# Optimization experiments

Measured on AMD Instinct MI355X. Metric: run time of the kernel, lower is better.

Reference implementation:

```python
import jax, jax.numpy as jnp
import numpy as np

N_NODES = 1500
N_EDGES = 12000
IN_FEAT = 512
HIDDEN = 64
OUT_FEAT = 32
HEADS = 8
NEG_SLOPE = 0.2  # DGL GATConv default leaky_relu slope


def setup_inputs() -> dict:
    key = jax.random.key(0)
    ks = jax.random.split(key, 16)

    def xav(k, shape, fan_in):
        return jax.random.normal(k, shape, jnp.float32) * (1.0 / np.sqrt(fan_in))

    return {
        "node": jax.random.normal(ks[0], (N_NODES, IN_FEAT), jnp.float32),
        "src": jax.random.randint(ks[1], (N_EDGES,), 0, N_NODES, jnp.int32),
        "dst": jax.random.randint(ks[2], (N_EDGES,), 0, N_NODES, jnp.int32),
        "W1": xav(ks[3], (IN_FEAT, HEADS * HIDDEN), IN_FEAT),
        "al1": xav(ks[4], (HEADS, HIDDEN), HIDDEN),
        "ar1": xav(ks[5], (HEADS, HIDDEN), HIDDEN),
        "b1": jnp.zeros((HEADS, HIDDEN), jnp.float32),
        "W2": xav(ks[6], (HIDDEN, HEADS * HIDDEN), HIDDEN),
        "al2": xav(ks[7], (HEADS, HIDDEN), HIDDEN),
        "ar2": xav(ks[8], (HEADS, HIDDEN), HIDDEN),
        "b2": jnp.zeros((HEADS, HIDDEN), jnp.float32),
        "W3": xav(ks[9], (HIDDEN, HEADS * OUT_FEAT), HIDDEN),
        "al3": xav(ks[10], (HEADS, OUT_FEAT), OUT_FEAT),
        "ar3": xav(ks[11], (HEADS, OUT_FEAT), OUT_FEAT),
        "b3": jnp.zeros((HEADS, OUT_FEAT), jnp.float32),
    }


def gat_layer(h, W, al, ar, b, src, dst, n_nodes):
    """DGL GATConv semantics: h has shape [N, *prefix, F_in]; output [N, *prefix, H, F_out]."""
    H, Fo = al.shape
    feat = (h @ W).reshape(h.shape[:-1] + (H, Fo))          # [N, *P, H, Fo]
    el = (feat * al).sum(-1)                                 # [N, *P, H]
    er = (feat * ar).sum(-1)                                 # [N, *P, H]
    e = jax.nn.leaky_relu(el[src] + er[dst], NEG_SLOPE)      # [E, *P, H]
    # numerically stable edge softmax over incoming edges of each dst node
    emax = jax.lax.stop_gradient(jax.ops.segment_max(e, dst, num_segments=n_nodes))
    ex = jnp.exp(e - emax[dst])
    den = jax.ops.segment_sum(ex, dst, num_segments=n_nodes)
    a = ex / den[dst]                                        # [E, *P, H]
    msg = a[..., None] * feat[src]                           # [E, *P, H, Fo]
    return jax.ops.segment_sum(msg, dst, num_segments=n_nodes) + b


def reference(node, src, dst, W1, al1, ar1, b1, W2, al2, ar2, b2, W3, al3, ar3, b3):
    n = node.shape[0]
    h = gat_layer(node, W1, al1, ar1, b1, src, dst, n)       # [N, 8, 64]
    h = jax.nn.gelu(h, approximate=False)
    h = gat_layer(h, W2, al2, ar2, b2, src, dst, n)          # [N, 8, 8, 64]
    h = jax.nn.gelu(h, approximate=False)
    return gat_layer(h, W3, al3, ar3, b3, src, dst, n)       # [N, 8, 8, 8, 32]
```

## Files before the change

kernel.cpp:

```cpp
#include <hip/hip_runtime.h>
#include <math.h>

#define N_NODES 1500
#define N_EDGES 12000
#define IN_FEAT 512
#define HIDDEN 64
#define OUT_FEAT 32
#define HEADS 8

typedef short bf16x8 __attribute__((ext_vector_type(8)));
typedef float f32x4 __attribute__((ext_vector_type(4)));

__device__ __forceinline__ unsigned short f2bf(float f) {
    unsigned u = __float_as_uint(f);
    u += 0x7fff + ((u >> 16) & 1);
    return (unsigned short)(u >> 16);
}
__device__ __forceinline__ float bf2f(unsigned short b) {
    return __uint_as_float(((unsigned)b) << 16);
}
__device__ __forceinline__ unsigned packbf(float a) {
    unsigned short hi = f2bf(a);
    unsigned short lo = f2bf(a - bf2f(hi));
    return (unsigned)hi | ((unsigned)lo << 16);
}
__device__ __forceinline__ float rdlane(float v, int c) {
    return __uint_as_float(__builtin_amdgcn_readlane(__float_as_uint(v), c));
}


__global__ void prep_kernel(const float* __restrict__ W2, const float* __restrict__ al2,
                            const float* __restrict__ ar2,
                            const float* __restrict__ W3, const float* __restrict__ al3,
                            const float* __restrict__ ar3,
                            float* __restrict__ aleff2, float* __restrict__ areff2,
                            float* __restrict__ aleff3, float* __restrict__ areff3,
                            float* __restrict__ W4t2, unsigned* __restrict__ wfrag3,
                            int* __restrict__ counts, int* __restrict__ cursor) {
    int i = blockIdx.x * blockDim.x + threadIdx.x;
    if (i < 1536) {
        if (i < N_NODES + 1) counts[i] = 0;
        return;
    }
    i -= 1536;
    if (i < 1536) {
        if (i < N_NODES) cursor[i] = 0;
        return;
    }
    i -= 1536;
    if (i < 1024) {
        int lr = i >> 9; i &= 511;
        int h = i >> 6, k = i & 63;
        const float* a = lr ? ar2 : al2;
        float s = 0.f;
        for (int f = 0; f < 64; ++f)
            s = fmaf(W2[(size_t)k * 512 + h * 64 + f], a[h * 64 + f], s);
        (lr ? areff2 : aleff2)[h * 64 + k] = s;
        return;
    }
    i -= 1024;
    if (i < 1024) {
        int lr = i >> 9; i &= 511;
        int h = i >> 6, k = i & 63;
        const float* a = lr ? ar3 : al3;
        float s = 0.f;
        for (int f = 0; f < 32; ++f)
            s = fmaf(W3[(size_t)k * 256 + h * 32 + f], a[h * 32 + f], s);
        (lr ? areff3 : aleff3)[h * 64 + k] = s;
        return;
    }
    i -= 1024;
    if (i < 16 * 512 * 4) {
        int kg = i >> 11, rem = i & 2047;
        int c = rem >> 2, j = rem & 3;
        W4t2[i] = W2[(size_t)(kg * 4 + j) * 512 + c];
        return;
    }
    i -= 16 * 512 * 4;
    if (i < 16384) {
        int j = i & 7, l = (i >> 3) & 63;
        int ks = (i >> 9) & 1, nt = (i >> 10) & 1, h = (i >> 11) & 7;
        int k = ks * 32 + (l >> 4) * 8 + j;
        int col = h * 32 + nt * 16 + (l & 15);
        wfrag3[i] = packbf(W3[(size_t)k * 256 + col]);
    }
}

__global__ void hist_kernel(const int* __restrict__ dst, int* __restrict__ counts) {
    int e = blockIdx.x * blockDim.x + threadIdx.x;
    if (e < N_EDGES) atomicAdd(&counts[dst[e]], 1);
}

__global__ void scan_kernel(const int* __restrict__ counts, int* __restrict__ row_ptr) {
    __shared__ int part[256];
    int t = threadIdx.x;
    const int CH = (N_NODES + 255) / 256;
    int base = t * CH;
    int loc[8];
    int s = 0;
    for (int i = 0; i < CH; ++i) {
        int idx = base + i;
        int v = (idx < N_NODES) ? counts[idx] : 0;
        loc[i] = s;
        s += v;
    }
    part[t] = s;
    __syncthreads();
    if (t == 0) {
        int a = 0;
        for (int i = 0; i < 256; ++i) { int v = part[i]; part[i] = a; a += v; }
        row_ptr[N_NODES] = a;
    }
    __syncthreads();
    int p0 = part[t];
    for (int i = 0; i < CH; ++i) {
        int idx = base + i;
        if (idx < N_NODES) row_ptr[idx] = p0 + loc[i];
    }
}

__global__ void scatter_kernel(const int* __restrict__ dst, const int* __restrict__ row_ptr,
                               int* __restrict__ cursor, int* __restrict__ tmp_eid) {
    int e = blockIdx.x * blockDim.x + threadIdx.x;
    if (e < N_EDGES) {
        int d = dst[e];
        int pos = row_ptr[d] + atomicAdd(&cursor[d], 1);
        tmp_eid[pos] = e;
    }
}

__global__ void sort_csr_kernel(const int* __restrict__ row_ptr, const int* __restrict__ tmp_eid,
                                const int* __restrict__ src, int* __restrict__ csr_src) {
    int wid = (blockIdx.x * blockDim.x + threadIdx.x) >> 6;
    int lane = threadIdx.x & 63;
    if (wid >= N_NODES) return;
    int r0 = row_ptr[wid], deg = row_ptr[wid + 1] - r0;
    for (int base = 0; base < deg; base += 64) {
        int i = base + lane;
        int my = (i < deg) ? tmp_eid[r0 + i] : 0x7fffffff;
        int rank = 0;
        for (int b2 = 0; b2 < deg; b2 += 64) {
            int other = (b2 + lane < deg) ? tmp_eid[r0 + b2 + lane] : 0x7fffffff;
            int cnt2 = min(deg - b2, 64);
            for (int j = 0; j < cnt2; ++j) {
                int oj = __shfl(other, j);
                rank += (oj < my) ? 1 : 0;
            }
        }
        if (i < deg) csr_src[r0 + rank] = src[my];
    }
}


#define GM 32
#define GN 32
#define GK 32

__global__ __launch_bounds__(256) void gemm_f32(const float* __restrict__ A,
                                                const float* __restrict__ B,
                                                float* __restrict__ C,
                                                int M, int N, int K) {
    __shared__ float As[GK][GM + 2];
    __shared__ float Bs[GK][GN + 2];
    int t = threadIdx.x;
    int col0 = blockIdx.x * GN, row0 = blockIdx.y * GM;
    int tx = t & 15, ty = t >> 4;
    int am = t >> 3, ak = (t & 7) * 4;
    int bk = t >> 3, bn = (t & 7) * 4;
    float acc[2][2] = {};
    for (int k0 = 0; k0 < K; k0 += GK) {
        int gr = row0 + am;
        float4 av = (gr < M) ? *(const float4*)&A[(size_t)gr * K + k0 + ak]
                             : make_float4(0.f, 0.f, 0.f, 0.f);
        float4 bv = *(const float4*)&B[(size_t)(k0 + bk) * N + col0 + bn];
        __syncthreads();
        As[ak + 0][am] = av.x; As[ak + 1][am] = av.y;
        As[ak + 2][am] = av.z; As[ak + 3][am] = av.w;
        *(float4*)&Bs[bk][bn] = bv;
        __syncthreads();
        #pragma unroll
        for (int kk = 0; kk < GK; ++kk) {
            float2 a2 = *(const float2*)&As[kk][ty * 2];
            float2 b2 = *(const float2*)&Bs[kk][tx * 2];
            acc[0][0] = fmaf(a2.x, b2.x, acc[0][0]);
            acc[0][1] = fmaf(a2.x, b2.y, acc[0][1]);
            acc[1][0] = fmaf(a2.y, b2.x, acc[1][0]);
            acc[1][1] = fmaf(a2.y, b2.y, acc[1][1]);
        }
    }
    #pragma unroll
    for (int i = 0; i < 2; ++i) {
        int gr = row0 + ty * 2 + i;
        if (gr < M) {
            float2 v = make_float2(acc[i][0], acc[i][1]);
            *(float2*)&C[(size_t)gr * N + col0 + tx * 2] = v;
        }
    }
}


__global__ void elr_feat_kernel(const float* __restrict__ feat, const float* __restrict__ al,
                                const float* __restrict__ ar, float* __restrict__ el,
                                float* __restrict__ er, int RH) {
    int idx = blockIdx.x * blockDim.x + threadIdx.x;
    if (idx >= RH) return;
    int h = idx & (HEADS - 1);
    const float* fp = feat + (size_t)idx * HIDDEN;
    float sl = 0.f, sr = 0.f;
    for (int f = 0; f < HIDDEN; ++f) {
        float v = fp[f];
        sl = fmaf(v, al[h * HIDDEN + f], sl);
        sr = fmaf(v, ar[h * HIDDEN + f], sr);
    }
    el[idx] = sl;
    er[idx] = sr;
}

__global__ void elr_row_kernel(const float* __restrict__ X, const float* __restrict__ alv,
                               const float* __restrict__ arv, float* __restrict__ el,
                               float* __restrict__ er, int R) {
    int r = blockIdx.x * blockDim.x + threadIdx.x;
    if (r >= R) return;
    const float4* x4 = (const float4*)(X + (size_t)r * 64);
    float sl[8] = {}, sr[8] = {};
    for (int kg = 0; kg < 16; ++kg) {
        float4 xv = x4[kg];
        #pragma unroll
        for (int h = 0; h < 8; ++h) {
            float4 a = *(const float4*)&alv[h * 64 + kg * 4];
            float4 b = *(const float4*)&arv[h * 64 + kg * 4];
            sl[h] = fmaf(xv.x, a.x, fmaf(xv.y, a.y, fmaf(xv.z, a.z, fmaf(xv.w, a.w, sl[h]))));
            sr[h] = fmaf(xv.x, b.x, fmaf(xv.y, b.y, fmaf(xv.z, b.z, fmaf(xv.w, b.w, sr[h]))));
        }
    }
    float* elp = el + (size_t)r * 8;
    float* erp = er + (size_t)r * 8;
    #pragma unroll
    for (int h = 0; h < 8; ++h) { elp[h] = sl[h]; erp[h] = sr[h]; }
}

__device__ __forceinline__ float gelu_exact(float v) {
    return 0.5f * v * (1.0f + erff(v * 0.70710678118654752440f));
}

__global__ __launch_bounds__(256) void agg_l1(
    const float* __restrict__ feat, const float* __restrict__ el, const float* __restrict__ er,
    const float* __restrict__ bias, const int* __restrict__ row_ptr,
    const int* __restrict__ csr_src, float* __restrict__ out) {
    int n = blockIdx.x;
    int t = threadIdx.x, wv = t >> 6, lane = t & 63;
    int h0 = 2 * wv;
    int r0 = row_ptr[n], deg = row_ptr[n + 1] - r0;
    float2 erv = *(const float2*)&er[n * 8 + h0];
    float den0 = 0.f, den1 = 0.f, a0 = 0.f, a1 = 0.f;
    for (int i = 0; i < deg; ++i) {
        int s = csr_src[r0 + i];
        float2 elv = *(const float2*)&el[s * 8 + h0];
        float x0 = feat[((size_t)s * 8 + h0) * 64 + lane];
        float x1 = feat[((size_t)s * 8 + h0 + 1) * 64 + lane];
        float e0 = elv.x + erv.x; e0 = e0 > 0.f ? e0 : 0.2f * e0;
        float e1 = elv.y + erv.y; e1 = e1 > 0.f ? e1 : 0.2f * e1;
        float w0 = __expf(e0), w1 = __expf(e1);
        den0 += w0; den1 += w1;
        a0 = fmaf(w0, x0, a0);
        a1 = fmaf(w1, x1, a1);
    }
    float i0 = deg ? 1.f / den0 : 0.f;
    float i1 = deg ? 1.f / den1 : 0.f;
    float v0 = a0 * i0 + bias[h0 * 64 + lane];
    float v1 = a1 * i1 + bias[(h0 + 1) * 64 + lane];
    out[((size_t)n * 8 + h0) * 64 + lane] = gelu_exact(v0);
    out[((size_t)n * 8 + h0 + 1) * 64 + lane] = gelu_exact(v1);
}

template <int FOUT, bool GELU, int P>
__global__ __launch_bounds__(256, 4) void agg_fused4(
    const float* __restrict__ X,
    const float* __restrict__ el, const float* __restrict__ er,
    const float* __restrict__ W4t,
    const float* __restrict__ bias,
    const int* __restrict__ row_ptr, const int* __restrict__ csr_src,
    float* __restrict__ out)
{
    constexpr int TOT = 8 * FOUT;
    constexpr int KSPLIT = 2;
    constexpr int KGPT = 8;
    constexpr int FELEM = (FOUT == 32) ? 2 : 4;
    constexpr int FQn = FOUT / FELEM;
    constexpr int TPK = 8 * FQn;
    constexpr int FQ4 = FOUT / 4;
    constexpr int PTS = FOUT + 4;
    constexpr int WPFL = (KSPLIT * 64 * PTS > 64 * 64) ? KSPLIT * 64 * PTS : 64 * 64;
    constexpr int GRPS = P / 8;
    constexpr int CHUNK = 64;

    int nb = blockIdx.x;
    int n = nb / GRPS, pg = nb - n * GRPS;
    int p0 = pg * 8;
    int r0 = row_ptr[n], deg = row_ptr[n + 1] - r0;
    int t = threadIdx.x, wv = t >> 6, lane = t & 63;

    __shared__ int src_s[CHUNK];
    __shared__ float inv_s[64];
    __shared__ float acc_s[8][8][68];
    __shared__ float wp_lds[WPFL];

    float agg0[8], agg1[8];
    #pragma unroll
    for (int h = 0; h < 8; ++h) { agg0[h] = 0.f; agg1[h] = 0.f; }
    float den = 0.f;

    int elbase_n = (n * P + p0) * 8;
    int pA = p0 + wv * 2;

    for (int c0 = 0; c0 < deg; c0 += CHUNK) {
        int cnt = min(deg - c0, CHUNK);
        __syncthreads();
        if (t < cnt) src_s[t] = csr_src[r0 + c0 + t];
        for (int j = t; j < cnt * 64; j += 256) {
            int i = j >> 6, plh = j & 63;
            int s = csr_src[r0 + c0 + i];
            float e = el[(s * P + p0) * 8 + plh] + er[elbase_n + plh];
            e = e > 0.f ? e : 0.2f * e;
            wp_lds[i * 64 + plh] = __expf(e);
        }
        __syncthreads();
        if (t < 64) {
            for (int i = 0; i < cnt; ++i) den += wp_lds[i * 64 + t];
        }
        auto edge_fma = [&](int i) {
            int s = src_s[i];
            const float* wp = &wp_lds[i * 64 + wv * 16];
            float4 w0 = *(const float4*)wp;
            float4 w1 = *(const float4*)(wp + 4);
            float4 w2 = *(const float4*)(wp + 8);
            float4 w3 = *(const float4*)(wp + 12);
            int xb = (s * P + pA) * 64 + lane;
            float xv0 = X[xb];
            float xv1 = X[xb + 64];
            agg0[0] = fmaf(w0.x, xv0, agg0[0]);
            agg0[1] = fmaf(w0.y, xv0, agg0[1]);
            agg0[2] = fmaf(w0.z, xv0, agg0[2]);
            agg0[3] = fmaf(w0.w, xv0, agg0[3]);
            agg0[4] = fmaf(w1.x, xv0, agg0[4]);
            agg0[5] = fmaf(w1.y, xv0, agg0[5]);
            agg0[6] = fmaf(w1.z, xv0, agg0[6]);
            agg0[7] = fmaf(w1.w, xv0, agg0[7]);
            agg1[0] = fmaf(w2.x, xv1, agg1[0]);
            agg1[1] = fmaf(w2.y, xv1, agg1[1]);
            agg1[2] = fmaf(w2.z, xv1, agg1[2]);
            agg1[3] = fmaf(w2.w, xv1, agg1[3]);
            agg1[4] = fmaf(w3.x, xv1, agg1[4]);
            agg1[5] = fmaf(w3.y, xv1, agg1[5]);
            agg1[6] = fmaf(w3.z, xv1, agg1[6]);
            agg1[7] = fmaf(w3.w, xv1, agg1[7]);
        };
        int i = 0;
        for (; i + 2 <= cnt; i += 2) { edge_fma(i); edge_fma(i + 1); }
        if (i < cnt) edge_fma(i);
    }
    if (t < 64) inv_s[t] = deg ? 1.f / den : 0.f;
    __syncthreads();
    {
        int pl0 = wv * 2;
        #pragma unroll
        for (int h = 0; h < 8; ++h) {
            acc_s[pl0][h][lane] = agg0[h] * inv_s[pl0 * 8 + h];
            acc_s[pl0 + 1][h][lane] = agg1[h] * inv_s[pl0 * 8 + 8 + h];
        }
    }
    __syncthreads();

    {
        int kq = t / TPK;
        int rem = t - kq * TPK;
        int h = rem / FQn;
        int ft = rem - h * FQn;
        int f0 = ft * FELEM;
        float part[8][FELEM];
        #pragma unroll
        for (int pl = 0; pl < 8; ++pl)
            #pragma unroll
            for (int j = 0; j < FELEM; ++j) part[pl][j] = 0.f;
        #pragma unroll
        for (int kk = 0; kk < KGPT; ++kk) {
            int kg = kq * KGPT + kk;
            float4 wr[FELEM];
            #pragma unroll
            for (int j = 0; j < FELEM; ++j)
                wr[j] = *(const float4*)&W4t[(size_t)(kg * TOT + h * FOUT + f0 + j) * 4];
            #pragma unroll
            for (int pl = 0; pl < 8; ++pl) {
                float4 a4 = *(const float4*)&acc_s[pl][h][kg * 4];
                #pragma unroll
                for (int j = 0; j < FELEM; ++j)
                    part[pl][j] = fmaf(a4.x, wr[j].x, fmaf(a4.y, wr[j].y,
                                  fmaf(a4.z, wr[j].z, fmaf(a4.w, wr[j].w, part[pl][j]))));
            }
        }
        #pragma unroll
        for (int pl = 0; pl < 8; ++pl) {
            float* dstp = &wp_lds[((kq * 8 + pl) * 8 + h) * PTS + f0];
            if (FELEM == 4)
                *(float4*)dstp = make_float4(part[pl][0], part[pl][1], part[pl][2], part[pl][3]);
            else
                *(float2*)dstp = make_float2(part[pl][0], part[pl][1]);
        }
    }
    __syncthreads();

    {
        constexpr int NQ = 2 * TOT;
        for (int q = t; q < NQ; q += 256) {
            int pl = q / (TOT / 4);
            int rem = q - pl * (TOT / 4);
            int h = rem / FQ4, fq = rem - h * FQ4;
            int f0 = fq * 4;
            float4 acc4 = *(const float4*)&wp_lds[((0 * 8 + pl) * 8 + h) * PTS + f0];
            #pragma unroll
            for (int kq = 1; kq < KSPLIT; ++kq) {
                float4 pv = *(const float4*)&wp_lds[((kq * 8 + pl) * 8 + h) * PTS + f0];
                acc4.x += pv.x; acc4.y += pv.y; acc4.z += pv.z; acc4.w += pv.w;
            }
            float4 b4 = *(const float4*)&bias[h * FOUT + f0];
            acc4.x += b4.x; acc4.y += b4.y; acc4.z += b4.z; acc4.w += b4.w;
            if (GELU) {
                acc4.x = gelu_exact(acc4.x); acc4.y = gelu_exact(acc4.y);
                acc4.z = gelu_exact(acc4.z); acc4.w = gelu_exact(acc4.w);
            }
            *(float4*)&out[(size_t)(n * P + p0 + pl) * TOT + h * FOUT + f0] = acc4;
        }
    }
}

__global__ __launch_bounds__(256, 4) void agg_mfma5(
    const float* __restrict__ X,
    const float* __restrict__ el, const float* __restrict__ er,
    const unsigned* __restrict__ wfrag,
    const float* __restrict__ bias,
    const int* __restrict__ row_ptr, const int* __restrict__ csr_src,
    float* __restrict__ out)
{
    int nb = blockIdx.x;
    int n = nb >> 2, pg = nb & 3;
    int p0 = pg * 16;
    int r0 = row_ptr[n], deg = row_ptr[n + 1] - r0;
    int t = threadIdx.x, wv = t >> 6, lane = t & 63;
    int pA = p0 + wv * 4;

    __shared__ unsigned accP[8][16][68];

    int c = lane & 31;
    float erv = er[(n * 64 + pA) * 8 + c];

    float agg[4][8];
    #pragma unroll
    for (int q = 0; q < 4; ++q)
        #pragma unroll
        for (int h = 0; h < 8; ++h) agg[q][h] = 0.f;
    float den_half = 0.f;

    for (int it = 0; it < deg; it += 2) {
        int s0 = csr_src[r0 + it];
        bool v1 = (it + 1 < deg);
        int s1 = v1 ? csr_src[r0 + it + 1] : s0;
        int sw = (lane < 32) ? s0 : s1;
        float e = el[(sw * 64 + pA) * 8 + c] + erv;
        e = e > 0.f ? e : 0.2f * e;
        if (lane >= 32 && !v1) e = -1e30f;
        float w = __expf(e);
        den_half += w;
        int xb0 = (s0 * 64 + pA) * 64 + lane;
        int xb1 = (s1 * 64 + pA) * 64 + lane;
        float xv0[4], xv1[4];
        #pragma unroll
        for (int q = 0; q < 4; ++q) xv0[q] = X[xb0 + q * 64];
        #pragma unroll
        for (int q = 0; q < 4; ++q) xv1[q] = X[xb1 + q * 64];
        #pragma unroll
        for (int q = 0; q < 4; ++q) {
            #pragma unroll
            for (int h = 0; h < 8; ++h) {
                float w0 = rdlane(w, q * 8 + h);
                float w1 = rdlane(w, 32 + q * 8 + h);
                agg[q][h] = fmaf(w0, xv0[q], agg[q][h]);
                agg[q][h] = fmaf(w1, xv1[q], agg[q][h]);
            }
        }
    }
    float den = den_half + __shfl(den_half, lane ^ 32);
    float inv = deg ? 1.f / den : 0.f;

    #pragma unroll
    for (int q = 0; q < 4; ++q) {
        int pl = wv * 4 + q;
        #pragma unroll
        for (int h = 0; h < 8; ++h) {
            float iv = rdlane(inv, q * 8 + h);
            accP[h][pl][lane] = packbf(agg[q][h] * iv);
        }
    }
    __syncthreads();

    int m16 = lane & 15, g = lane >> 4;
    #pragma unroll
    for (int hh = 0; hh < 2; ++hh) {
        int h = wv * 2 + hh;
        bf16x8 a_hi[2], a_lo[2];
        #pragma unroll
        for (int ks = 0; ks < 2; ++ks) {
            const unsigned* ap = &accP[h][m16][ks * 32 + g * 8];
            uint4 q0 = *(const uint4*)ap;
            uint4 q1 = *(const uint4*)(ap + 4);
            a_hi[ks][0] = (short)(q0.x & 0xffffu); a_lo[ks][0] = (short)(q0.x >> 16);
            a_hi[ks][1] = (short)(q0.y & 0xffffu); a_lo[ks][1] = (short)(q0.y >> 16);
            a_hi[ks][2] = (short)(q0.z & 0xffffu); a_lo[ks][2] = (short)(q0.z >> 16);
            a_hi[ks][3] = (short)(q0.w & 0xffffu); a_lo[ks][3] = (short)(q0.w >> 16);
            a_hi[ks][4] = (short)(q1.x & 0xffffu); a_lo[ks][4] = (short)(q1.x >> 16);
            a_hi[ks][5] = (short)(q1.y & 0xffffu); a_lo[ks][5] = (short)(q1.y >> 16);
            a_hi[ks][6] = (short)(q1.z & 0xffffu); a_lo[ks][6] = (short)(q1.z >> 16);
            a_hi[ks][7] = (short)(q1.w & 0xffffu); a_lo[ks][7] = (short)(q1.w >> 16);
        }
        #pragma unroll
        for (int nt = 0; nt < 2; ++nt) {
            f32x4 D = {0.f, 0.f, 0.f, 0.f};
            #pragma unroll
            for (int ks = 0; ks < 2; ++ks) {
                const unsigned* bp = &wfrag[(size_t)(((h * 2 + nt) * 2 + ks) * 64 + lane) * 8];
                uint4 w0 = *(const uint4*)bp;
                uint4 w1 = *(const uint4*)(bp + 4);
                bf16x8 b_hi, b_lo;
                b_hi[0] = (short)(w0.x & 0xffffu); b_lo[0] = (short)(w0.x >> 16);
                b_hi[1] = (short)(w0.y & 0xffffu); b_lo[1] = (short)(w0.y >> 16);
                b_hi[2] = (short)(w0.z & 0xffffu); b_lo[2] = (short)(w0.z >> 16);
                b_hi[3] = (short)(w0.w & 0xffffu); b_lo[3] = (short)(w0.w >> 16);
                b_hi[4] = (short)(w1.x & 0xffffu); b_lo[4] = (short)(w1.x >> 16);
                b_hi[5] = (short)(w1.y & 0xffffu); b_lo[5] = (short)(w1.y >> 16);
                b_hi[6] = (short)(w1.z & 0xffffu); b_lo[6] = (short)(w1.z >> 16);
                b_hi[7] = (short)(w1.w & 0xffffu); b_lo[7] = (short)(w1.w >> 16);
                D = __builtin_amdgcn_mfma_f32_16x16x32_bf16(a_hi[ks], b_hi, D, 0, 0, 0);
                D = __builtin_amdgcn_mfma_f32_16x16x32_bf16(a_hi[ks], b_lo, D, 0, 0, 0);
                D = __builtin_amdgcn_mfma_f32_16x16x32_bf16(a_lo[ks], b_hi, D, 0, 0, 0);
            }
            float bv = bias[h * 32 + nt * 16 + m16];
            size_t ob = ((size_t)(n * 64) + p0 + g * 4) * 256 + h * 32 + nt * 16 + m16;
            out[ob]       = D[0] + bv;
            out[ob + 256] = D[1] + bv;
            out[ob + 512] = D[2] + bv;
            out[ob + 768] = D[3] + bv;
        }
    }
}


extern "C" void kernel_launch(void* const* d_in, const int* in_sizes, int n_in,
                              void* d_out, int out_size, void* d_ws, size_t ws_size,
                              hipStream_t stream) {
    const float* node = (const float*)d_in[0];
    const int* src = (const int*)d_in[1];
    const int* dst = (const int*)d_in[2];
    const float* W1 = (const float*)d_in[3];
    const float* al1 = (const float*)d_in[4];
    const float* ar1 = (const float*)d_in[5];
    const float* b1 = (const float*)d_in[6];
    const float* W2 = (const float*)d_in[7];
    const float* al2 = (const float*)d_in[8];
    const float* ar2 = (const float*)d_in[9];
    const float* b2 = (const float*)d_in[10];
    const float* W3 = (const float*)d_in[11];
    const float* al3 = (const float*)d_in[12];
    const float* ar3 = (const float*)d_in[13];
    const float* b3 = (const float*)d_in[14];
    float* out = (float*)d_out;

    char* ws = (char*)d_ws;
    size_t off = 0;
    auto alloc = [&](size_t nb) -> char* {
        char* q = ws + off;
        off += (nb + 255) & ~(size_t)255;
        return q;
    };
    int* counts   = (int*)alloc((N_NODES + 1) * sizeof(int));
    int* cursor   = (int*)alloc(N_NODES * sizeof(int));
    int* row_ptr  = (int*)alloc((N_NODES + 1) * sizeof(int));
    int* tmp_eid  = (int*)alloc(N_EDGES * sizeof(int));
    int* csr_src  = (int*)alloc(N_EDGES * sizeof(int));
    float* feat1  = (float*)alloc((size_t)N_NODES * 8 * 64 * 4);
    float* el1    = (float*)alloc((size_t)N_NODES * 8 * 4);
    float* er1    = (float*)alloc((size_t)N_NODES * 8 * 4);
    float* h1     = (float*)alloc((size_t)N_NODES * 8 * 64 * 4);
    float* aleff2 = (float*)alloc(8 * 64 * 4);
    float* areff2 = (float*)alloc(8 * 64 * 4);
    float* el2    = (float*)alloc((size_t)N_NODES * 8 * 8 * 4);
    float* er2    = (float*)alloc((size_t)N_NODES * 8 * 8 * 4);
    float* h2     = (float*)alloc((size_t)N_NODES * 64 * 64 * 4);
    float* aleff3 = (float*)alloc(8 * 64 * 4);
    float* areff3 = (float*)alloc(8 * 64 * 4);
    float* el3    = (float*)alloc((size_t)N_NODES * 64 * 8 * 4);
    float* er3    = (float*)alloc((size_t)N_NODES * 64 * 8 * 4);
    float* W4t2   = (float*)alloc((size_t)16 * 512 * 4 * 4);
    unsigned* wfrag3 = (unsigned*)alloc((size_t)16384 * 4);

    const int PREP_T = 1536 + 1536 + 1024 + 1024 + 16 * 512 * 4 + 16384;
    prep_kernel<<<(PREP_T + 255) / 256, 256, 0, stream>>>(
        W2, al2, ar2, W3, al3, ar3, aleff2, areff2, aleff3, areff3, W4t2, wfrag3,
        counts, cursor);

    hist_kernel<<<(N_EDGES + 255) / 256, 256, 0, stream>>>(dst, counts);
    scan_kernel<<<1, 256, 0, stream>>>(counts, row_ptr);
    scatter_kernel<<<(N_EDGES + 255) / 256, 256, 0, stream>>>(dst, row_ptr, cursor, tmp_eid);
    sort_csr_kernel<<<(N_NODES * 64 + 255) / 256, 256, 0, stream>>>(row_ptr, tmp_eid, src, csr_src);

    dim3 g1((512 + GN - 1) / GN, (N_NODES + GM - 1) / GM);
    gemm_f32<<<g1, 256, 0, stream>>>(node, W1, feat1, N_NODES, 512, IN_FEAT);
    elr_feat_kernel<<<(N_NODES * 8 + 255) / 256, 256, 0, stream>>>(feat1, al1, ar1, el1, er1, N_NODES * 8);
    agg_l1<<<N_NODES, 256, 0, stream>>>(feat1, el1, er1, b1, row_ptr, csr_src, h1);

    elr_row_kernel<<<(N_NODES * 8 + 255) / 256, 256, 0, stream>>>(h1, aleff2, areff2, el2, er2, N_NODES * 8);
    agg_fused4<64, true, 8><<<N_NODES, 256, 0, stream>>>(h1, el2, er2, W4t2, b2, row_ptr, csr_src, h2);

    elr_row_kernel<<<(N_NODES * 64 + 255) / 256, 256, 0, stream>>>(h2, aleff3, areff3, el3, er3, N_NODES * 64);
    agg_mfma5<<<N_NODES * 4, 256, 0, stream>>>(h2, el3, er3, wfrag3, b3, row_ptr, csr_src, out);
}
```

Before: 177.4 us.

## Wave-register edge index broadcast, 4-edge unrolling, split bf16 weight planes, block remap

All three aggregation kernels now load a chunk of up to 64 source indices into one register per lane and broadcast them with readlane, replacing repeated global or LDS index loads. The layer-3 aggregation processes four edges per iteration so more gathers are in flight. Its B fragments now come as pre-split hi/lo bf16 planes and load directly as vectors, with no unpacking in the kernel. Block indices are remapped so that consecutive blocks handle different p-groups. The extra unrolling raises register pressure, and the remap changes L2 locality in ways that are hard to predict.

```diff
diff --git a/kernel.cpp b/kernel.cpp
--- a/kernel.cpp
+++ b/kernel.cpp
@@ -24,7 +24,7 @@
     unsigned short lo = f2bf(a - bf2f(hi));
     return (unsigned)hi | ((unsigned)lo << 16);
 }
-__device__ __forceinline__ float rdlane(float v, int c) {
+__device__ __forceinline__ float rdlanef(float v, int c) {
     return __uint_as_float(__builtin_amdgcn_readlane(__float_as_uint(v), c));
 }
 
@@ -35,7 +35,8 @@
                             const float* __restrict__ ar3,
                             float* __restrict__ aleff2, float* __restrict__ areff2,
                             float* __restrict__ aleff3, float* __restrict__ areff3,
-                            float* __restrict__ W4t2, unsigned* __restrict__ wfrag3,
+                            float* __restrict__ W4t2,
+                            unsigned* __restrict__ wfhi, unsigned* __restrict__ wflo,
                             int* __restrict__ counts, int* __restrict__ cursor) {
     int i = blockIdx.x * blockDim.x + threadIdx.x;
     if (i < 1536) {
@@ -78,11 +79,21 @@
     }
     i -= 16 * 512 * 4;
     if (i < 16384) {
-        int j = i & 7, l = (i >> 3) & 63;
-        int ks = (i >> 9) & 1, nt = (i >> 10) & 1, h = (i >> 11) & 7;
-        int k = ks * 32 + (l >> 4) * 8 + j;
+        int plane = i >> 13;
+        int rem = i & 8191;
+        int j2 = rem & 3, l = (rem >> 2) & 63;
+        int ks = (rem >> 8) & 1, nt = (rem >> 9) & 1, h = (rem >> 10) & 7;
         int col = h * 32 + nt * 16 + (l & 15);
-        wfrag3[i] = packbf(W3[(size_t)k * 256 + col]);
+        int kb = ks * 32 + (l >> 4) * 8 + 2 * j2;
+        unsigned parts[2];
+        #pragma unroll
+        for (int q = 0; q < 2; ++q) {
+            float w = W3[(size_t)(kb + q) * 256 + col];
+            unsigned short hi = f2bf(w);
+            parts[q] = plane ? (unsigned)f2bf(w - bf2f(hi)) : (unsigned)hi;
+        }
+        unsigned word = parts[0] | (parts[1] << 16);
+        (plane ? wflo : wfhi)[rem] = word;
     }
 }
 
@@ -253,17 +264,28 @@
     int r0 = row_ptr[n], deg = row_ptr[n + 1] - r0;
     float2 erv = *(const float2*)&er[n * 8 + h0];
     float den0 = 0.f, den1 = 0.f, a0 = 0.f, a1 = 0.f;
-    for (int i = 0; i < deg; ++i) {
-        int s = csr_src[r0 + i];
-        float2 elv = *(const float2*)&el[s * 8 + h0];
-        float x0 = feat[((size_t)s * 8 + h0) * 64 + lane];
-        float x1 = feat[((size_t)s * 8 + h0 + 1) * 64 + lane];
-        float e0 = elv.x + erv.x; e0 = e0 > 0.f ? e0 : 0.2f * e0;
-        float e1 = elv.y + erv.y; e1 = e1 > 0.f ? e1 : 0.2f * e1;
-        float w0 = __expf(e0), w1 = __expf(e1);
-        den0 += w0; den1 += w1;
-        a0 = fmaf(w0, x0, a0);
-        a1 = fmaf(w1, x1, a1);
+    for (int c0 = 0; c0 < deg; c0 += 64) {
+        int cnt = min(deg - c0, 64);
+        int src_r = (lane < cnt) ? csr_src[r0 + c0 + lane] : 0;
+        auto do_edge = [&](int s) {
+            float2 elv = *(const float2*)&el[s * 8 + h0];
+            float x0 = feat[((size_t)s * 8 + h0) * 64 + lane];
+            float x1 = feat[((size_t)s * 8 + h0 + 1) * 64 + lane];
+            float e0 = elv.x + erv.x; e0 = e0 > 0.f ? e0 : 0.2f * e0;
+            float e1 = elv.y + erv.y; e1 = e1 > 0.f ? e1 : 0.2f * e1;
+            float w0 = __expf(e0), w1 = __expf(e1);
+            den0 += w0; den1 += w1;
+            a0 = fmaf(w0, x0, a0);
+            a1 = fmaf(w1, x1, a1);
+        };
+        int i = 0;
+        for (; i + 2 <= cnt; i += 2) {
+            int s0 = __builtin_amdgcn_readlane(src_r, i);
+            int s1 = __builtin_amdgcn_readlane(src_r, i + 1);
+            do_edge(s0);
+            do_edge(s1);
+        }
+        if (i < cnt) do_edge(__builtin_amdgcn_readlane(src_r, i));
     }
     float i0 = deg ? 1.f / den0 : 0.f;
     float i1 = deg ? 1.f / den1 : 0.f;
@@ -300,7 +322,6 @@
     int r0 = row_ptr[n], deg = row_ptr[n + 1] - r0;
     int t = threadIdx.x, wv = t >> 6, lane = t & 63;
 
-    __shared__ int src_s[CHUNK];
     __shared__ float inv_s[64];
     __shared__ float acc_s[8][8][68];
     __shared__ float wp_lds[WPFL];
@@ -312,24 +333,25 @@
 
     int elbase_n = (n * P + p0) * 8;
     int pA = p0 + wv * 2;
+    float erv_t = er[elbase_n + lane];
 
     for (int c0 = 0; c0 < deg; c0 += CHUNK) {
         int cnt = min(deg - c0, CHUNK);
+        int src_r = (lane < cnt) ? csr_src[r0 + c0 + lane] : 0;
         __syncthreads();
-        if (t < cnt) src_s[t] = csr_src[r0 + c0 + t];
         for (int j = t; j < cnt * 64; j += 256) {
-            int i = j >> 6, plh = j & 63;
-            int s = csr_src[r0 + c0 + i];
-            float e = el[(s * P + p0) * 8 + plh] + er[elbase_n + plh];
+            int i = j >> 6;
+            int s = __builtin_amdgcn_readlane(src_r, i);
+            float e = el[(s * P + p0) * 8 + lane] + erv_t;
             e = e > 0.f ? e : 0.2f * e;
-            wp_lds[i * 64 + plh] = __expf(e);
+            wp_lds[i * 64 + lane] = __expf(e);
         }
         __syncthreads();
         if (t < 64) {
             for (int i = 0; i < cnt; ++i) den += wp_lds[i * 64 + t];
         }
         auto edge_fma = [&](int i) {
-            int s = src_s[i];
+            int s = __builtin_amdgcn_readlane(src_r, i);
             const float* wp = &wp_lds[i * 64 + wv * 16];
             float4 w0 = *(const float4*)wp;
             float4 w1 = *(const float4*)(wp + 4);
@@ -436,13 +458,14 @@
 __global__ __launch_bounds__(256, 4) void agg_mfma5(
     const float* __restrict__ X,
     const float* __restrict__ el, const float* __restrict__ er,
-    const unsigned* __restrict__ wfrag,
+    const unsigned* __restrict__ wfhi, const unsigned* __restrict__ wflo,
     const float* __restrict__ bias,
     const int* __restrict__ row_ptr, const int* __restrict__ csr_src,
     float* __restrict__ out)
 {
-    int nb = blockIdx.x;
-    int n = nb >> 2, pg = nb & 3;
+    int b = blockIdx.x;
+    int w = (b & 7) * 750 + (b >> 3);
+    int pg = w / N_NODES, n = w - pg * N_NODES;
     int p0 = pg * 16;
     int r0 = row_ptr[n], deg = row_ptr[n + 1] - r0;
     int t = threadIdx.x, wv = t >> 6, lane = t & 63;
@@ -460,31 +483,49 @@
         for (int h = 0; h < 8; ++h) agg[q][h] = 0.f;
     float den_half = 0.f;
 
-    for (int it = 0; it < deg; it += 2) {
-        int s0 = csr_src[r0 + it];
-        bool v1 = (it + 1 < deg);
-        int s1 = v1 ? csr_src[r0 + it + 1] : s0;
-        int sw = (lane < 32) ? s0 : s1;
-        float e = el[(sw * 64 + pA) * 8 + c] + erv;
-        e = e > 0.f ? e : 0.2f * e;
-        if (lane >= 32 && !v1) e = -1e30f;
-        float w = __expf(e);
-        den_half += w;
-        int xb0 = (s0 * 64 + pA) * 64 + lane;
-        int xb1 = (s1 * 64 + pA) * 64 + lane;
-        float xv0[4], xv1[4];
-        #pragma unroll
-        for (int q = 0; q < 4; ++q) xv0[q] = X[xb0 + q * 64];
-        #pragma unroll
-        for (int q = 0; q < 4; ++q) xv1[q] = X[xb1 + q * 64];
-        #pragma unroll
-        for (int q = 0; q < 4; ++q) {
-            #pragma unroll
-            for (int h = 0; h < 8; ++h) {
-                float w0 = rdlane(w, q * 8 + h);
-                float w1 = rdlane(w, 32 + q * 8 + h);
-                agg[q][h] = fmaf(w0, xv0[q], agg[q][h]);
-                agg[q][h] = fmaf(w1, xv1[q], agg[q][h]);
+    for (int c0 = 0; c0 < deg; c0 += 64) {
+        int cnt = min(deg - c0, 64);
+        int src_r = (lane < cnt) ? csr_src[r0 + c0 + lane] : 0;
+        for (int it = 0; it < cnt; it += 4) {
+            int i1 = min(it + 1, cnt - 1), i2 = min(it + 2, cnt - 1), i3 = min(it + 3, cnt - 1);
+            int s0 = __builtin_amdgcn_readlane(src_r, it);
+            int s1 = __builtin_amdgcn_readlane(src_r, i1);
+            int s2 = __builtin_amdgcn_readlane(src_r, i2);
+            int s3 = __builtin_amdgcn_readlane(src_r, i3);
+            bool v1 = it + 1 < cnt, v2 = it + 2 < cnt, v3 = it + 3 < cnt;
+            int sA = (lane < 32) ? s0 : s1;
+            int sB = (lane < 32) ? s2 : s3;
+            float eA = el[(sA * 64 + pA) * 8 + c] + erv;
+            float eB = el[(sB * 64 + pA) * 8 + c] + erv;
+            eA = eA > 0.f ? eA : 0.2f * eA;
+            eB = eB > 0.f ? eB : 0.2f * eB;
+            if (lane >= 32 && !v1) eA = -1e30f;
+            if (lane < 32 && !v2) eB = -1e30f;
+            if (lane >= 32 && !v3) eB = -1e30f;
+            float wA = __expf(eA), wB = __expf(eB);
+            den_half += wA + wB;
+            int xb0 = (s0 * 64 + pA) * 64 + lane;
+            int xb1 = (s1 * 64 + pA) * 64 + lane;
+            int xb2 = (s2 * 64 + pA) * 64 + lane;
+            int xb3 = (s3 * 64 + pA) * 64 + lane;
+            float x0[4], x1[4], x2[4], x3[4];
+            #pragma unroll
+            for (int q = 0; q < 4; ++q) x0[q] = X[xb0 + q * 64];
+            #pragma unroll
+            for (int q = 0; q < 4; ++q) x1[q] = X[xb1 + q * 64];
+            #pragma unroll
+            for (int q = 0; q < 4; ++q) x2[q] = X[xb2 + q * 64];
+            #pragma unroll
+            for (int q = 0; q < 4; ++q) x3[q] = X[xb3 + q * 64];
+            #pragma unroll
+            for (int q = 0; q < 4; ++q) {
+                #pragma unroll
+                for (int h = 0; h < 8; ++h) {
+                    agg[q][h] = fmaf(rdlanef(wA, q * 8 + h), x0[q], agg[q][h]);
+                    agg[q][h] = fmaf(rdlanef(wA, 32 + q * 8 + h), x1[q], agg[q][h]);
+                    agg[q][h] = fmaf(rdlanef(wB, q * 8 + h), x2[q], agg[q][h]);
+                    agg[q][h] = fmaf(rdlanef(wB, 32 + q * 8 + h), x3[q], agg[q][h]);
+                }
             }
         }
     }
@@ -496,7 +537,7 @@
         int pl = wv * 4 + q;
         #pragma unroll
         for (int h = 0; h < 8; ++h) {
-            float iv = rdlane(inv, q * 8 + h);
+            float iv = rdlanef(inv, q * 8 + h);
             accP[h][pl][lane] = packbf(agg[q][h] * iv);
         }
     }
@@ -526,18 +567,9 @@
             f32x4 D = {0.f, 0.f, 0.f, 0.f};
             #pragma unroll
             for (int ks = 0; ks < 2; ++ks) {
-                const unsigned* bp = &wfrag[(size_t)(((h * 2 + nt) * 2 + ks) * 64 + lane) * 8];
-                uint4 w0 = *(const uint4*)bp;
-                uint4 w1 = *(const uint4*)(bp + 4);
-                bf16x8 b_hi, b_lo;
-                b_hi[0] = (short)(w0.x & 0xffffu); b_lo[0] = (short)(w0.x >> 16);
-                b_hi[1] = (short)(w0.y & 0xffffu); b_lo[1] = (short)(w0.y >> 16);
-                b_hi[2] = (short)(w0.z & 0xffffu); b_lo[2] = (short)(w0.z >> 16);
-                b_hi[3] = (short)(w0.w & 0xffffu); b_lo[3] = (short)(w0.w >> 16);
-                b_hi[4] = (short)(w1.x & 0xffffu); b_lo[4] = (short)(w1.x >> 16);
-                b_hi[5] = (short)(w1.y & 0xffffu); b_lo[5] = (short)(w1.y >> 16);
-                b_hi[6] = (short)(w1.z & 0xffffu); b_lo[6] = (short)(w1.z >> 16);
-                b_hi[7] = (short)(w1.w & 0xffffu); b_lo[7] = (short)(w1.w >> 16);
+                size_t fb = (size_t)(((h * 2 + nt) * 2 + ks) * 64 + lane) * 4;
+                bf16x8 b_hi = *(const bf16x8*)&wfhi[fb];
+                bf16x8 b_lo = *(const bf16x8*)&wflo[fb];
                 D = __builtin_amdgcn_mfma_f32_16x16x32_bf16(a_hi[ks], b_hi, D, 0, 0, 0);
                 D = __builtin_amdgcn_mfma_f32_16x16x32_bf16(a_hi[ks], b_lo, D, 0, 0, 0);
                 D = __builtin_amdgcn_mfma_f32_16x16x32_bf16(a_lo[ks], b_hi, D, 0, 0, 0);
@@ -599,11 +631,12 @@
     float* el3    = (float*)alloc((size_t)N_NODES * 64 * 8 * 4);
     float* er3    = (float*)alloc((size_t)N_NODES * 64 * 8 * 4);
     float* W4t2   = (float*)alloc((size_t)16 * 512 * 4 * 4);
-    unsigned* wfrag3 = (unsigned*)alloc((size_t)16384 * 4);
+    unsigned* wfhi = (unsigned*)alloc((size_t)8192 * 4);
+    unsigned* wflo = (unsigned*)alloc((size_t)8192 * 4);
 
     const int PREP_T = 1536 + 1536 + 1024 + 1024 + 16 * 512 * 4 + 16384;
     prep_kernel<<<(PREP_T + 255) / 256, 256, 0, stream>>>(
-        W2, al2, ar2, W3, al3, ar3, aleff2, areff2, aleff3, areff3, W4t2, wfrag3,
+        W2, al2, ar2, W3, al3, ar3, aleff2, areff2, aleff3, areff3, W4t2, wfhi, wflo,
         counts, cursor);
 
     hist_kernel<<<(N_EDGES + 255) / 256, 256, 0, stream>>>(dst, counts);
@@ -620,5 +653,5 @@
     agg_fused4<64, true, 8><<<N_NODES, 256, 0, stream>>>(h1, el2, er2, W4t2, b2, row_ptr, csr_src, h2);
 
     elr_row_kernel<<<(N_NODES * 64 + 255) / 256, 256, 0, stream>>>(h2, aleff3, areff3, el3, er3, N_NODES * 64);
-    agg_mfma5<<<N_NODES * 4, 256, 0, stream>>>(h2, el3, er3, wfrag3, b3, row_ptr, csr_src, out);
-}
+    agg_mfma5<<<N_NODES * 4, 256, 0, stream>>>(h2, el3, er3, wfhi, wflo, b3, row_ptr, csr_src, out);
+}
```

After: 176.3 us. Within noise of the previous version (-0.6%).
